# Kernel tuning notes

Measured on AMD Instinct MI355X. Metric: run time of the kernel, lower is better.

The kernel has to match this reference:

```python
import jax, jax.numpy as jnp
import numpy as np

N = 100000
E = 1600000
F_IN, F_HID, F_OUT = 128, 32, 2


def setup_inputs() -> dict:
    key = jax.random.key(0)
    k1, k2, k3, k4 = jax.random.split(key, 4)
    x = jax.random.normal(k1, (N, F_IN), dtype=jnp.float32)
    edge_index = jax.random.randint(k2, (2, E), 0, N, dtype=jnp.int64)
    # Glorot-style init like torch_geometric GCNConv
    W1 = jax.random.normal(k3, (F_IN, F_HID), dtype=jnp.float32) * (1.0 / np.sqrt(F_IN))
    b1 = jnp.zeros((F_HID,), dtype=jnp.float32)
    W2 = jax.random.normal(k4, (F_HID, F_OUT), dtype=jnp.float32) * (1.0 / np.sqrt(F_HID))
    b2 = jnp.zeros((F_OUT,), dtype=jnp.float32)
    return {"x": x, "edge_index": edge_index, "W1": W1, "b1": b1, "W2": W2, "b2": b2}


def _gcn_conv(x, row, col, norm, W, b):
    # GCNConv: transform, then normalized aggregate (source -> target), then bias
    h = x @ W                                   # [N, F_out]
    msg = norm[:, None] * h[row]                # gather + scale, [E+N, F_out]
    out = jax.ops.segment_sum(msg, col, num_segments=N)  # scatter-add to targets
    return out + b


def reference(x, edge_index, W1, b1, W2, b2):
    # add self-loops (GCNConv default)
    loops = jnp.arange(N, dtype=edge_index.dtype)
    row = jnp.concatenate([edge_index[0], loops])
    col = jnp.concatenate([edge_index[1], loops])
    # symmetric normalization: deg^{-1/2}[row] * deg^{-1/2}[col], deg = in-degree w/ self-loops
    deg = jax.ops.segment_sum(jnp.ones_like(col, dtype=x.dtype), col, num_segments=N)
    dinv = jnp.where(deg > 0, jax.lax.rsqrt(deg), 0.0)
    norm = dinv[row] * dinv[col]                # [E+N]

    h = _gcn_conv(x, row, col, norm, W1, b1)
    h = jax.nn.relu(h)
    h = _gcn_conv(h, row, col, norm, W2, b2)
    return jax.nn.log_softmax(h, axis=1)
```

## Files before the change

### kernel.cpp

```cpp
#include <hip/hip_runtime.h>
#include <hip/hip_bf16.h>
#include <math.h>
#include <stdint.h>


#define GNN_N 100000
#define GNN_E 1600000
#define NBUCK 391
#define CAP 4608
#define CHB 4096

typedef float fx2 __attribute__((ext_vector_type(2)));
typedef short short8x __attribute__((ext_vector_type(8)));
typedef float f32x4 __attribute__((ext_vector_type(4)));

__device__ inline uint16_t bf16_bits(float f) {
    uint32_t u = __float_as_uint(f);
    return (uint16_t)((u + 0x7fffu + ((u >> 16) & 1u)) >> 16);
}

__global__ __launch_bounds__(256) void k_bucket(const int* __restrict__ row,
                                                const int* __restrict__ col,
                                                int* __restrict__ bucket_fill,
                                                uint32_t* __restrict__ slab, int e) {
    __shared__ int hist[NBUCK];
    __shared__ int base[NBUCK];
    const int tid = threadIdx.x;
    const int e0 = blockIdx.x * CHB;
    const int m = min(CHB, e - e0);
    const bool full = (m == CHB);

    for (int i = tid; i < NBUCK; i += 256) hist[i] = 0;

    int cc[16], rr[16], pp[16];
    if (full) {
        const int4* c4 = (const int4*)(col + e0);
        const int4* r4 = (const int4*)(row + e0);
        #pragma unroll
        for (int t = 0; t < 4; ++t) {
            int4 c = c4[tid + t * 256];
            int4 r = r4[tid + t * 256];
            cc[t * 4 + 0] = c.x; cc[t * 4 + 1] = c.y;
            cc[t * 4 + 2] = c.z; cc[t * 4 + 3] = c.w;
            rr[t * 4 + 0] = r.x; rr[t * 4 + 1] = r.y;
            rr[t * 4 + 2] = r.z; rr[t * 4 + 3] = r.w;
        }
        __syncthreads();
        #pragma unroll
        for (int t = 0; t < 16; ++t)
            pp[t] = atomicAdd(&hist[cc[t] >> 8], 1);
    } else {
        __syncthreads();
        #pragma unroll
        for (int t = 0; t < 16; ++t) {
            int i = tid + t * 256;
            if (i < m) {
                cc[t] = col[e0 + i];
                rr[t] = row[e0 + i];
                pp[t] = atomicAdd(&hist[cc[t] >> 8], 1);
            }
        }
    }
    __syncthreads();
    for (int i = tid; i < NBUCK; i += 256) {
        int bb = (i + blockIdx.x * 131) % NBUCK;
        base[bb] = atomicAdd(&bucket_fill[bb], hist[bb]);
    }
    __syncthreads();
    if (full) {
        #pragma unroll
        for (int t = 0; t < 16; ++t) {
            int b = cc[t] >> 8;
            int p = base[b] + pp[t];
            if (p < CAP)
                slab[(size_t)b * CAP + p] = ((uint32_t)rr[t] << 8) | (uint32_t)(cc[t] & 255);
        }
    } else {
        #pragma unroll
        for (int t = 0; t < 16; ++t) {
            int i = tid + t * 256;
            if (i < m) {
                int b = cc[t] >> 8;
                int p = base[b] + pp[t];
                if (p < CAP)
                    slab[(size_t)b * CAP + p] = ((uint32_t)rr[t] << 8) | (uint32_t)(cc[t] & 255);
            }
        }
    }
}

__global__ __launch_bounds__(512) void k_fine(const uint32_t* __restrict__ slab,
                                              const int* __restrict__ bucket_fill,
                                              int* __restrict__ sorted_row,
                                              int* __restrict__ offsets,
                                              float* __restrict__ dinv, int n) {
    __shared__ int hist[256];
    __shared__ int excl[256];
    __shared__ int wsum[4];
    __shared__ int s_gbase;
    __shared__ uint32_t stage[CAP];
    const int tid = threadIdx.x;
    const int b0 = blockIdx.x * 2;
    const int lane = tid & 63, wave = tid >> 6;

    if (blockIdx.x == gridDim.x - 1 && tid == 511) offsets[n] = GNN_E;

    if (tid < 64) {
        int s = 0;
        for (int i = tid; i < b0; i += 64) s += bucket_fill[i];
        #pragma unroll
        for (int m = 32; m >= 1; m >>= 1) s += __shfl_xor(s, m);
        if (tid == 0) s_gbase = s;
    }
    __syncthreads();
    int gbase = s_gbase;

    for (int pass = 0; pass < 2; ++pass) {
        const int b = b0 + pass;
        if (b >= NBUCK) break;
        const int nb = min(bucket_fill[b], CAP);
        const uint32_t* sl = slab + (size_t)b * CAP;

        if (tid < 256) hist[tid] = 0;
        __syncthreads();
        uint32_t uu[9];
        int pp[9];
        #pragma unroll
        for (int j = 0; j < 9; ++j) {
            int i = tid + j * 512;
            if (i < nb) {
                uint32_t u = sl[i];
                uu[j] = u;
                pp[j] = atomicAdd(&hist[u & 255u], 1);
            }
        }
        __syncthreads();
        int v = 0, inc = 0;
        if (tid < 256) {
            v = hist[tid];
            inc = v;
            #pragma unroll
            for (int d = 1; d < 64; d <<= 1) {
                int t = __shfl_up(inc, d);
                if (lane >= d) inc += t;
            }
            if (lane == 63) wsum[wave] = inc;
        }
        __syncthreads();
        if (tid == 0) {
            int a = 0;
            #pragma unroll
            for (int w = 0; w < 4; ++w) { int t = wsum[w]; wsum[w] = a; a += t; }
        }
        __syncthreads();
        if (tid < 256) {
            int ex = inc - v + wsum[wave];
            excl[tid] = ex;
            int c = b * 256 + tid;
            if (c < n) {
                offsets[c] = gbase + ex;
                dinv[c] = rsqrtf((float)(v + 1));
            }
        }
        __syncthreads();
        #pragma unroll
        for (int j = 0; j < 9; ++j) {
            int i = tid + j * 512;
            if (i < nb)
                stage[excl[uu[j] & 255u] + pp[j]] = uu[j] >> 8;
        }
        __syncthreads();
        for (int i = tid; i < nb; i += 512)
            sorted_row[gbase + i] = (int)stage[i];
        gbase += nb;
        __syncthreads();
    }
}

#define XPAD 136
__global__ __launch_bounds__(256) void k_matmul1(const float* __restrict__ x,
                                                 const float* __restrict__ W1,
                                                 const float* __restrict__ dinv,
                                                 uint32_t* __restrict__ h1q, int n) {
    __shared__ uint16_t xs[64 * XPAD];
    __shared__ uint16_t w1t[32 * XPAD];
    const int tid = threadIdx.x;
    const int nodeBase = blockIdx.x * 64;

    for (int i = tid; i < 4096; i += 256) {
        int k = i >> 5, c = i & 31;
        w1t[c * XPAD + k] = bf16_bits(W1[i]);
    }
    {
        const float4* x4 = (const float4*)x;
        for (int i = tid; i < 64 * 32; i += 256) {
            int node = i >> 5;
            int k4 = i & 31;
            float4 v = make_float4(0.f, 0.f, 0.f, 0.f);
            if (nodeBase + node < n)
                v = x4[(size_t)(nodeBase + node) * 32 + k4];
            int b = node * XPAD + k4 * 4;
            xs[b + 0] = bf16_bits(v.x); xs[b + 1] = bf16_bits(v.y);
            xs[b + 2] = bf16_bits(v.z); xs[b + 3] = bf16_bits(v.w);
        }
    }
    __syncthreads();

    const int wave = tid >> 6;
    const int lane = tid & 63;
    const int nn = lane & 15;
    const int quad = lane >> 4;
    f32x4 acc0 = {0.f, 0.f, 0.f, 0.f};
    f32x4 acc1 = {0.f, 0.f, 0.f, 0.f};
    const int xrow = (wave * 16 + nn) * XPAD;
    #pragma unroll
    for (int s = 0; s < 4; ++s) {
        const int kof = s * 32 + quad * 8;
        short8x bfrag = *(const short8x*)&xs[xrow + kof];
        short8x a0 = *(const short8x*)&w1t[nn * XPAD + kof];
        short8x a1 = *(const short8x*)&w1t[(16 + nn) * XPAD + kof];
        acc0 = __builtin_amdgcn_mfma_f32_16x16x32_bf16(a0, bfrag, acc0, 0, 0, 0);
        acc1 = __builtin_amdgcn_mfma_f32_16x16x32_bf16(a1, bfrag, acc1, 0, 0, 0);
    }
    const int gn = nodeBase + wave * 16 + nn;
    if (gn < n) {
        float d = dinv[gn];
        int w0 = 0, w1 = 0;
        w0 = __builtin_amdgcn_cvt_pk_fp8_f32(acc0[0] * d, acc0[1] * d, w0, false);
        w0 = __builtin_amdgcn_cvt_pk_fp8_f32(acc0[2] * d, acc0[3] * d, w0, true);
        w1 = __builtin_amdgcn_cvt_pk_fp8_f32(acc1[0] * d, acc1[1] * d, w1, false);
        w1 = __builtin_amdgcn_cvt_pk_fp8_f32(acc1[2] * d, acc1[3] * d, w1, true);
        h1q[(size_t)gn * 8 + quad] = (uint32_t)w0;
        h1q[(size_t)gn * 8 + 4 + quad] = (uint32_t)w1;
    }
}

__device__ inline void fp8x16_acc(float* a, uint4 u) {
    fx2 p;
    p = __builtin_amdgcn_cvt_pk_f32_fp8(u.x, false); a[0] += p.x;  a[1] += p.y;
    p = __builtin_amdgcn_cvt_pk_f32_fp8(u.x, true);  a[2] += p.x;  a[3] += p.y;
    p = __builtin_amdgcn_cvt_pk_f32_fp8(u.y, false); a[4] += p.x;  a[5] += p.y;
    p = __builtin_amdgcn_cvt_pk_f32_fp8(u.y, true);  a[6] += p.x;  a[7] += p.y;
    p = __builtin_amdgcn_cvt_pk_f32_fp8(u.z, false); a[8] += p.x;  a[9] += p.y;
    p = __builtin_amdgcn_cvt_pk_f32_fp8(u.z, true);  a[10] += p.x; a[11] += p.y;
    p = __builtin_amdgcn_cvt_pk_f32_fp8(u.w, false); a[12] += p.x; a[13] += p.y;
    p = __builtin_amdgcn_cvt_pk_f32_fp8(u.w, true);  a[14] += p.x; a[15] += p.y;
}

__global__ __launch_bounds__(256) void k_gather1(const int* __restrict__ offsets,
                                                 const int* __restrict__ sorted_row,
                                                 const uint32_t* __restrict__ h1q,
                                                 const float* __restrict__ dinv,
                                                 const float* __restrict__ b1,
                                                 const float* __restrict__ W2,
                                                 float* __restrict__ h2s, int n) {
    __shared__ float sb1[32];
    __shared__ float sW2[64];
    const int tid = threadIdx.x;
    if (tid < 32) sb1[tid] = b1[tid];
    else if (tid < 96) sW2[tid - 32] = W2[tid - 32];
    __syncthreads();

    const int l = tid & 1;
    const int node = blockIdx.x * 128 + (tid >> 1);
    if (node >= n) return;
    const uint4* h4 = (const uint4*)h1q;
    float acc[16], acc2[16];
    #pragma unroll
    for (int j = 0; j < 16; ++j) { acc[j] = 0.f; acc2[j] = 0.f; }
    fp8x16_acc(acc, h4[(size_t)node * 2 + l]);
    const int start = offsets[node];
    const int deg = offsets[node + 1] - start;
    const int* sr = sorted_row + start;
    int k = 0;
    for (; k + 8 <= deg; k += 8) {
        int r[8];
        uint4 u[8];
        #pragma unroll
        for (int t = 0; t < 8; ++t) r[t] = sr[k + t];
        #pragma unroll
        for (int t = 0; t < 8; ++t) u[t] = h4[(size_t)r[t] * 2 + l];
        #pragma unroll
        for (int t = 0; t < 8; ++t) fp8x16_acc((t & 1) ? acc2 : acc, u[t]);
    }
    for (; k + 2 <= deg; k += 2) {
        int ra = sr[k], rb = sr[k + 1];
        uint4 ua = h4[(size_t)ra * 2 + l];
        uint4 ub = h4[(size_t)rb * 2 + l];
        fp8x16_acc(acc, ua);
        fp8x16_acc(acc2, ub);
    }
    if (k < deg)
        fp8x16_acc(acc, h4[(size_t)sr[k] * 2 + l]);
    #pragma unroll
    for (int j = 0; j < 16; ++j) acc[j] += acc2[j];

    const float dc = dinv[node];
    const int f0 = l * 16;
    float s0 = 0.f, s1 = 0.f;
    #pragma unroll
    for (int j = 0; j < 16; ++j) {
        float a = fmaxf(dc * acc[j] + sb1[f0 + j], 0.f);
        s0 += a * sW2[(f0 + j) * 2];
        s1 += a * sW2[(f0 + j) * 2 + 1];
    }
    s0 += __shfl_xor(s0, 1);
    s1 += __shfl_xor(s1, 1);
    if (l == 0) ((float2*)h2s)[node] = make_float2(dc * s0, dc * s1);
}

__global__ __launch_bounds__(256) void k_gather2(const int* __restrict__ offsets,
                                                 const int* __restrict__ sorted_row,
                                                 const float* __restrict__ h2s,
                                                 const float* __restrict__ dinv,
                                                 const float* __restrict__ b2,
                                                 float* __restrict__ out, int n) {
    const int tid = threadIdx.x;
    const int l = tid & 3;
    const int node = blockIdx.x * 64 + (tid >> 2);
    if (node >= n) return;
    const float2* h2 = (const float2*)h2s;
    float sx = 0.f, sy = 0.f;
    if (l == 0) { float2 s = h2[node]; sx = s.x; sy = s.y; }
    const int start = offsets[node];
    const int deg = offsets[node + 1] - start;
    for (int k = l; k < deg; k += 4) {
        float2 v = h2[sorted_row[start + k]];
        sx += v.x; sy += v.y;
    }
    sx += __shfl_xor(sx, 1); sx += __shfl_xor(sx, 2);
    sy += __shfl_xor(sy, 1); sy += __shfl_xor(sy, 2);
    if (l == 0) {
        float d = dinv[node];
        float v0 = d * sx + b2[0];
        float v1 = d * sy + b2[1];
        float m = fmaxf(v0, v1);
        float lg = m + logf(expf(v0 - m) + expf(v1 - m));
        ((float2*)out)[node] = make_float2(v0 - lg, v1 - lg);
    }
}

extern "C" void kernel_launch(void* const* d_in, const int* in_sizes, int n_in,
                              void* d_out, int out_size, void* d_ws, size_t ws_size,
                              hipStream_t stream) {
    const float* x  = (const float*)d_in[0];
    const int*   ei = (const int*)d_in[1];
    const float* W1 = (const float*)d_in[2];
    const float* b1 = (const float*)d_in[3];
    const float* W2 = (const float*)d_in[4];
    const float* b2 = (const float*)d_in[5];
    float* out = (float*)d_out;
    char* ws = (char*)d_ws;

    const int N = GNN_N, E = GNN_E;
    const int* row = ei;
    const int* col = ei + GNN_E;

    float*    dinv        = (float*)    ws;
    int*      offsets     = (int*)     (ws + 4ull *  100000);
    int*      bucket_fill = (int*)     (ws + 4ull *  200512);
    int*      sorted_row  = (int*)     (ws + 4ull *  201024);
    float*    h2s         = (float*)   (ws + 4ull * 1801024);
    uint32_t* h1q         = (uint32_t*)(ws + 4ull * 2001024);
    uint32_t* slab        = (uint32_t*)(ws + 4ull * 2801024);

    hipMemsetAsync(bucket_fill, 0, NBUCK * sizeof(int), stream);

    k_bucket <<<(E + CHB - 1) / CHB, 256, 0, stream>>>(row, col, bucket_fill, slab, E);
    k_fine   <<<(NBUCK + 1) / 2, 512, 0, stream>>>(slab, bucket_fill, sorted_row, offsets, dinv, N);
    k_matmul1<<<(N + 63) / 64, 256, 0, stream>>>(x, W1, dinv, h1q, N);
    k_gather1<<<(N + 127) / 128, 256, 0, stream>>>(offsets, sorted_row, h1q, dinv, b1, W2, h2s, N);
    k_gather2<<<(N + 63) / 64, 256, 0, stream>>>(offsets, sorted_row, h2s, dinv, b2, out, N);
}
```

Baseline: 164.6 us.

## Split LDS histograms, drop fine-sort staging, use bf16 layer-2 features

The bucketing kernel moves to 512 threads with two per-wave-parity shared histograms, which is meant to cut LDS atomic contention. The fine sort uses the same split histograms and writes sorted rows straight to global memory instead of through a shared staging buffer. The layer-2 intermediate is packed as bf16x2 instead of float2, halving the bytes read by the second gather. The bf16 storage costs some precision in the layer-2 sums, and the direct global scatter writes are less coalesced.

After: 168.1 us. +2.1%, slower.

```diff
diff --git a/kernel.cpp b/kernel.cpp
--- a/kernel.cpp
+++ b/kernel.cpp
@@ -18,28 +18,36 @@
     uint32_t u = __float_as_uint(f);
     return (uint16_t)((u + 0x7fffu + ((u >> 16) & 1u)) >> 16);
 }
-
-__global__ __launch_bounds__(256) void k_bucket(const int* __restrict__ row,
+__device__ inline uint32_t pack_bf16x2(float a, float b) {
+    return (uint32_t)bf16_bits(a) | ((uint32_t)bf16_bits(b) << 16);
+}
+__device__ inline float bf_lo(uint32_t u) { return __uint_as_float(u << 16); }
+__device__ inline float bf_hi(uint32_t u) { return __uint_as_float(u & 0xffff0000u); }
+
+__global__ __launch_bounds__(512) void k_bucket(const int* __restrict__ row,
                                                 const int* __restrict__ col,
                                                 int* __restrict__ bucket_fill,
                                                 uint32_t* __restrict__ slab, int e) {
-    __shared__ int hist[NBUCK];
+    __shared__ int histA[NBUCK];
+    __shared__ int histB[NBUCK];
     __shared__ int base[NBUCK];
     const int tid = threadIdx.x;
     const int e0 = blockIdx.x * CHB;
     const int m = min(CHB, e - e0);
     const bool full = (m == CHB);
-
-    for (int i = tid; i < NBUCK; i += 256) hist[i] = 0;
-
-    int cc[16], rr[16], pp[16];
+    const int isB = (tid >> 6) & 1;
+    int* myh = isB ? histB : histA;
+
+    for (int i = tid; i < NBUCK; i += 512) { histA[i] = 0; histB[i] = 0; }
+
+    int cc[8], rr[8], pp[8];
     if (full) {
         const int4* c4 = (const int4*)(col + e0);
         const int4* r4 = (const int4*)(row + e0);
         #pragma unroll
-        for (int t = 0; t < 4; ++t) {
-            int4 c = c4[tid + t * 256];
-            int4 r = r4[tid + t * 256];
+        for (int t = 0; t < 2; ++t) {
+            int4 c = c4[tid + t * 512];
+            int4 r = r4[tid + t * 512];
             cc[t * 4 + 0] = c.x; cc[t * 4 + 1] = c.y;
             cc[t * 4 + 2] = c.z; cc[t * 4 + 3] = c.w;
             rr[t * 4 + 0] = r.x; rr[t * 4 + 1] = r.y;
@@ -47,41 +55,41 @@
         }
         __syncthreads();
         #pragma unroll
-        for (int t = 0; t < 16; ++t)
-            pp[t] = atomicAdd(&hist[cc[t] >> 8], 1);
+        for (int t = 0; t < 8; ++t)
+            pp[t] = atomicAdd(&myh[cc[t] >> 8], 1);
     } else {
         __syncthreads();
         #pragma unroll
-        for (int t = 0; t < 16; ++t) {
-            int i = tid + t * 256;
+        for (int t = 0; t < 8; ++t) {
+            int i = tid + t * 512;
             if (i < m) {
                 cc[t] = col[e0 + i];
                 rr[t] = row[e0 + i];
-                pp[t] = atomicAdd(&hist[cc[t] >> 8], 1);
-            }
-        }
-    }
-    __syncthreads();
-    for (int i = tid; i < NBUCK; i += 256) {
+                pp[t] = atomicAdd(&myh[cc[t] >> 8], 1);
+            }
+        }
+    }
+    __syncthreads();
+    for (int i = tid; i < NBUCK; i += 512) {
         int bb = (i + blockIdx.x * 131) % NBUCK;
-        base[bb] = atomicAdd(&bucket_fill[bb], hist[bb]);
+        base[bb] = atomicAdd(&bucket_fill[bb], histA[bb] + histB[bb]);
     }
     __syncthreads();
     if (full) {
         #pragma unroll
-        for (int t = 0; t < 16; ++t) {
+        for (int t = 0; t < 8; ++t) {
             int b = cc[t] >> 8;
-            int p = base[b] + pp[t];
+            int p = base[b] + (isB ? histA[b] : 0) + pp[t];
             if (p < CAP)
                 slab[(size_t)b * CAP + p] = ((uint32_t)rr[t] << 8) | (uint32_t)(cc[t] & 255);
         }
     } else {
         #pragma unroll
-        for (int t = 0; t < 16; ++t) {
-            int i = tid + t * 256;
+        for (int t = 0; t < 8; ++t) {
+            int i = tid + t * 512;
             if (i < m) {
                 int b = cc[t] >> 8;
-                int p = base[b] + pp[t];
+                int p = base[b] + (isB ? histA[b] : 0) + pp[t];
                 if (p < CAP)
                     slab[(size_t)b * CAP + p] = ((uint32_t)rr[t] << 8) | (uint32_t)(cc[t] & 255);
             }
@@ -94,14 +102,16 @@
                                               int* __restrict__ sorted_row,
                                               int* __restrict__ offsets,
                                               float* __restrict__ dinv, int n) {
-    __shared__ int hist[256];
+    __shared__ int histA[256];
+    __shared__ int histB[256];
     __shared__ int excl[256];
     __shared__ int wsum[4];
     __shared__ int s_gbase;
-    __shared__ uint32_t stage[CAP];
     const int tid = threadIdx.x;
     const int b0 = blockIdx.x * 2;
     const int lane = tid & 63, wave = tid >> 6;
+    const int isB = (tid >> 6) & 1;
+    int* myh = isB ? histB : histA;
 
     if (blockIdx.x == gridDim.x - 1 && tid == 511) offsets[n] = GNN_E;
 
@@ -121,7 +131,7 @@
         const int nb = min(bucket_fill[b], CAP);
         const uint32_t* sl = slab + (size_t)b * CAP;
 
-        if (tid < 256) hist[tid] = 0;
+        if (tid < 256) { histA[tid] = 0; histB[tid] = 0; }
         __syncthreads();
         uint32_t uu[9];
         int pp[9];
@@ -131,13 +141,13 @@
             if (i < nb) {
                 uint32_t u = sl[i];
                 uu[j] = u;
-                pp[j] = atomicAdd(&hist[u & 255u], 1);
+                pp[j] = atomicAdd(&myh[u & 255u], 1);
             }
         }
         __syncthreads();
         int v = 0, inc = 0;
         if (tid < 256) {
-            v = hist[tid];
+            v = histA[tid] + histB[tid];
             inc = v;
             #pragma unroll
             for (int d = 1; d < 64; d <<= 1) {
@@ -166,12 +176,12 @@
         #pragma unroll
         for (int j = 0; j < 9; ++j) {
             int i = tid + j * 512;
-            if (i < nb)
-                stage[excl[uu[j] & 255u] + pp[j]] = uu[j] >> 8;
-        }
-        __syncthreads();
-        for (int i = tid; i < nb; i += 512)
-            sorted_row[gbase + i] = (int)stage[i];
+            if (i < nb) {
+                int f = (int)(uu[j] & 255u);
+                int p = gbase + excl[f] + (isB ? histA[f] : 0) + pp[j];
+                sorted_row[p] = (int)(uu[j] >> 8);
+            }
+        }
         gbase += nb;
         __syncthreads();
     }
@@ -253,7 +263,7 @@
                                                  const float* __restrict__ dinv,
                                                  const float* __restrict__ b1,
                                                  const float* __restrict__ W2,
-                                                 float* __restrict__ h2s, int n) {
+                                                 uint32_t* __restrict__ h2b, int n) {
     __shared__ float sb1[32];
     __shared__ float sW2[64];
     const int tid = threadIdx.x;
@@ -306,12 +316,12 @@
     }
     s0 += __shfl_xor(s0, 1);
     s1 += __shfl_xor(s1, 1);
-    if (l == 0) ((float2*)h2s)[node] = make_float2(dc * s0, dc * s1);
+    if (l == 0) h2b[node] = pack_bf16x2(dc * s0, dc * s1);
 }
 
 __global__ __launch_bounds__(256) void k_gather2(const int* __restrict__ offsets,
                                                  const int* __restrict__ sorted_row,
-                                                 const float* __restrict__ h2s,
+                                                 const uint32_t* __restrict__ h2b,
                                                  const float* __restrict__ dinv,
                                                  const float* __restrict__ b2,
                                                  float* __restrict__ out, int n) {
@@ -319,14 +329,13 @@
     const int l = tid & 3;
     const int node = blockIdx.x * 64 + (tid >> 2);
     if (node >= n) return;
-    const float2* h2 = (const float2*)h2s;
     float sx = 0.f, sy = 0.f;
-    if (l == 0) { float2 s = h2[node]; sx = s.x; sy = s.y; }
+    if (l == 0) { uint32_t s = h2b[node]; sx = bf_lo(s); sy = bf_hi(s); }
     const int start = offsets[node];
     const int deg = offsets[node + 1] - start;
     for (int k = l; k < deg; k += 4) {
-        float2 v = h2[sorted_row[start + k]];
-        sx += v.x; sy += v.y;
+        uint32_t u = h2b[sorted_row[start + k]];
+        sx += bf_lo(u); sy += bf_hi(u);
     }
     sx += __shfl_xor(sx, 1); sx += __shfl_xor(sx, 2);
     sy += __shfl_xor(sy, 1); sy += __shfl_xor(sy, 2);
@@ -360,15 +369,15 @@
     int*      offsets     = (int*)     (ws + 4ull *  100000);
     int*      bucket_fill = (int*)     (ws + 4ull *  200512);
     int*      sorted_row  = (int*)     (ws + 4ull *  201024);
-    float*    h2s         = (float*)   (ws + 4ull * 1801024);
-    uint32_t* h1q         = (uint32_t*)(ws + 4ull * 2001024);
-    uint32_t* slab        = (uint32_t*)(ws + 4ull * 2801024);
+    uint32_t* h2b         = (uint32_t*)(ws + 4ull * 1801024);
+    uint32_t* h1q         = (uint32_t*)(ws + 4ull * 1901024);
+    uint32_t* slab        = (uint32_t*)(ws + 4ull * 2701024);
 
     hipMemsetAsync(bucket_fill, 0, NBUCK * sizeof(int), stream);
 
-    k_bucket <<<(E + CHB - 1) / CHB, 256, 0, stream>>>(row, col, bucket_fill, slab, E);
+    k_bucket <<<(E + CHB - 1) / CHB, 512, 0, stream>>>(row, col, bucket_fill, slab, E);
     k_fine   <<<(NBUCK + 1) / 2, 512, 0, stream>>>(slab, bucket_fill, sorted_row, offsets, dinv, N);
     k_matmul1<<<(N + 63) / 64, 256, 0, stream>>>(x, W1, dinv, h1q, N);
-    k_gather1<<<(N + 127) / 128, 256, 0, stream>>>(offsets, sorted_row, h1q, dinv, b1, W2, h2s, N);
-    k_gather2<<<(N + 63) / 64, 256, 0, stream>>>(offsets, sorted_row, h2s, dinv, b2, out, N);
-}
+    k_gather1<<<(N + 127) / 128, 256, 0, stream>>>(offsets, sorted_row, h1q, dinv, b1, W2, h2b, N);
+    k_gather2<<<(N + 63) / 64, 256, 0, stream>>>(offsets, sorted_row, h2b, dinv, b2, out, N);
+}
```
